# Performance work log

Measured on AMD Instinct MI355X. Metric: run time of the kernel, lower is better.

The kernel has to match this reference:

```python
import jax, jax.numpy as jnp
import numpy as np

EPS = 1e-8  # torch F.cosine_similarity default eps
NEG_INF = jnp.float32(-1e30)


def setup_inputs() -> dict:
    key = jax.random.key(0)
    k1, k2 = jax.random.split(key)
    N, M, D = 65536, 1024, 256
    embeddings = jax.random.normal(k1, (N, D), dtype=jnp.float32)
    prototypes = jax.random.normal(k2, (M, D), dtype=jnp.float32)
    counts = jnp.ones((M,), dtype=jnp.int64)  # all categories active
    return {"embeddings": embeddings, "prototypes": prototypes, "counts": counts}


def reference(embeddings, prototypes, counts):
    # Cosine similarity without materializing [N, M, D]:
    # sim[n, m] = <e_n, p_m> / max(||e_n|| * ||p_m||, eps)
    e_norm = jnp.linalg.norm(embeddings, axis=-1)            # [N]
    p_norm = jnp.linalg.norm(prototypes, axis=-1)            # [M]
    dots = jnp.einsum("nd,md->nm", embeddings, prototypes)   # [N, M]
    sim = dots / jnp.maximum(e_norm[:, None] * p_norm[None, :], EPS)
    # Mask inactive prototypes (counts == 0), matching `prototypes[active]`.
    active = counts > 0                                       # [M]
    sim = jnp.where(active[None, :], sim, NEG_INF)
    return jnp.argmax(sim, axis=-1)                           # [N] int
```

## Files before the change

### kernel.cpp

```cpp
#include <hip/hip_runtime.h>
#include <hip/hip_bf16.h>

typedef _Float16 f16x8 __attribute__((ext_vector_type(8)));
typedef float f32x4 __attribute__((ext_vector_type(4)));

#define TAU_Q 164
#define MASK_Q 2098790u

typedef const __attribute__((address_space(1))) void gas_void;
typedef __attribute__((address_space(3))) void las_void;

__device__ __forceinline__ void gload_lds16(const void* g, void* l) {
  __builtin_amdgcn_global_load_lds((gas_void*)g, (las_void*)l, 16, 0, 0);
}

__global__ __launch_bounds__(64) void prep_kernel(
    const float* __restrict__ P, const int* __restrict__ counts,
    float* __restrict__ q, int* __restrict__ wcount, f16x8* __restrict__ bhi) {
  const int m = blockIdx.x, lane = threadIdx.x;
  if (m == 0 && lane == 0) *wcount = 0;
  float4 v = *reinterpret_cast<const float4*>(P + (size_t)m * 256 + lane * 4);
  float s = v.x * v.x + v.y * v.y + v.z * v.z + v.w * v.w;
  for (int off = 32; off > 0; off >>= 1) s += __shfl_xor(s, off, 64);
  const float qm = (counts[m] > 0) ? (1.0f / sqrtf(s)) : 0.0f;
  if (lane == 0) q[m] = qm;
  if (lane < 32) {
    const int kg = lane;
    const float* src = P + (size_t)m * 256 + kg * 8;
    float4 v0 = *reinterpret_cast<const float4*>(src);
    float4 v1 = *reinterpret_cast<const float4*>(src + 4);
    float pe[8] = {v0.x, v0.y, v0.z, v0.w, v1.x, v1.y, v1.z, v1.w};
    f16x8 hi;
#pragma unroll
    for (int t = 0; t < 8; ++t) hi[t] = (_Float16)(pe[t] * qm);
    const int dst = ((m >> 4) * 8 + (kg >> 2)) * 64 + (kg & 3) * 16 + (m & 15);
    bhi[dst] = hi;
  }
}

__global__ __launch_bounds__(256) void screen_kernel(
    const float* __restrict__ E, const f16x8* __restrict__ bhi,
    int* __restrict__ out, int* __restrict__ wcount,
    int* __restrict__ wl, int wlcap) {
  __shared__ __align__(16) unsigned char ldsB[32768];

  const int tid = threadIdx.x;
  const int wave = tid >> 6, lane = tid & 63;
  const int g = lane >> 4, c = lane & 15;
  const int blockRow = blockIdx.x * 128;
  const char* bhiB = (const char*)bhi;

  auto stageB = [&](int b, int ch) {
#pragma unroll
    for (int i = 0; i < 4; ++i) {
      const int j = wave * 4 + i;
      gload_lds16(bhiB + ((size_t)ch << 14) + ((size_t)j << 10) + (size_t)lane * 16,
                  (char*)ldsB + (b << 14) + (j << 10));
    }
  };

  stageB(0, 0);

  f16x8 a[2][8];
#pragma unroll
  for (int fr = 0; fr < 2; ++fr) {
    const float* rowp = E + (size_t)(blockRow + wave * 32 + fr * 16 + c) * 256 + g * 8;
#pragma unroll
    for (int kc = 0; kc < 8; ++kc) {
      const float* p = rowp + kc * 32;
      float4 v0 = *reinterpret_cast<const float4*>(p);
      float4 v1 = *reinterpret_cast<const float4*>(p + 4);
      f16x8 h;
      h[0] = (_Float16)v0.x; h[1] = (_Float16)v0.y;
      h[2] = (_Float16)v0.z; h[3] = (_Float16)v0.w;
      h[4] = (_Float16)v1.x; h[5] = (_Float16)v1.y;
      h[6] = (_Float16)v1.z; h[7] = (_Float16)v1.w;
      a[fr][kc] = h;
    }
  }
  __syncthreads();

  unsigned t1[8], t2[8];
#pragma unroll
  for (int s = 0; s < 8; ++s) { t1[s] = 0u; t2[s] = 0u; }

#pragma unroll 1
  for (int ch = 0; ch < 32; ++ch) {
    const int buf = ch & 1;
    if (ch < 31) stageB(buf ^ 1, ch + 1);

    f32x4 acc[2][2];
#pragma unroll
    for (int fr = 0; fr < 2; ++fr)
#pragma unroll
      for (int fc = 0; fc < 2; ++fc) acc[fr][fc] = (f32x4){0.f, 0.f, 0.f, 0.f};

#pragma unroll
    for (int kc = 0; kc < 8; ++kc) {
      f16x8 bf[2];
#pragma unroll
      for (int fc = 0; fc < 2; ++fc) {
        const int j = fc * 8 + kc;
        bf[fc] = *reinterpret_cast<const f16x8*>(
            (const char*)ldsB + (buf << 14) + (j << 10) + (size_t)lane * 16);
      }
#pragma unroll
      for (int fr = 0; fr < 2; ++fr)
#pragma unroll
        for (int fc = 0; fc < 2; ++fc)
          acc[fr][fc] = __builtin_amdgcn_mfma_f32_16x16x32_f16(a[fr][kc], bf[fc], acc[fr][fc], 0, 0, 0);
    }

#pragma unroll
    for (int fc = 0; fc < 2; ++fc) {
      const unsigned mp = (unsigned)(1023 - (ch * 32 + fc * 16 + c));
#pragma unroll
      for (int fr = 0; fr < 2; ++fr)
#pragma unroll
        for (int reg = 0; reg < 4; ++reg) {
          const int s = fr * 4 + reg;
          const float v = acc[fr][fc][reg];
          const unsigned k = ((unsigned)fmaf(v, 32768.0f, 2097152.0f) << 10) | mp;
          const unsigned lo = (k < t1[s]) ? k : t1[s];
          t1[s] = (k > t1[s]) ? k : t1[s];
          t2[s] = (lo > t2[s]) ? lo : t2[s];
        }
    }

    __syncthreads();
  }

#pragma unroll
  for (int s = 0; s < 8; ++s) {
#pragma unroll
    for (int off = 1; off <= 8; off <<= 1) {
      const unsigned o1 = (unsigned)__shfl_xor((int)t1[s], off);
      const unsigned o2 = (unsigned)__shfl_xor((int)t2[s], off);
      const unsigned lo = (o1 < t1[s]) ? o1 : t1[s];
      t1[s] = (o1 > t1[s]) ? o1 : t1[s];
      const unsigned hi2 = (o2 > t2[s]) ? o2 : t2[s];
      t2[s] = (lo > hi2) ? lo : hi2;
    }
  }

  if (c == 0) {
#pragma unroll
    for (int s = 0; s < 8; ++s) {
      const int grow = blockRow + wave * 32 + (s >> 2) * 16 + g * 4 + (s & 3);
      const unsigned T1 = t1[s], T2 = t2[s];
      out[grow] = 1023 - (int)(T1 & 1023u);
      const unsigned iq1 = T1 >> 10, iq2 = T2 >> 10;
      if ((int)(iq1 - iq2) < TAU_Q || iq1 < MASK_Q) {
        const int p = atomicAdd(wcount, 1);
        if (p < wlcap) wl[p] = grow;
      }
    }
  }
}

__global__ __launch_bounds__(256) void rescue_kernel(
    const float* __restrict__ E, const float* __restrict__ P,
    const float* __restrict__ q, int* __restrict__ out,
    const int* __restrict__ wcount, const int* __restrict__ wl, int wlcap) {
  __shared__ float Elds[4][260];
  __shared__ int rowsS[4];
  __shared__ float wv[4][4];
  __shared__ int wm[4][4];

  const int tid = threadIdx.x;
  const int wave = tid >> 6, lane = tid & 63;
  int total = *wcount;
  if (total > wlcap) total = wlcap;

  for (int b0 = blockIdx.x * 4; b0 < total; b0 += gridDim.x * 4) {
    const int nb = min(4, total - b0);
    __syncthreads();
    if (tid < 4) rowsS[tid] = wl[b0 + (tid < nb ? tid : 0)];
    __syncthreads();
    {
      const int r = tid >> 6, k4 = tid & 63;
      *reinterpret_cast<float4*>(&Elds[r][k4 * 4]) =
          *reinterpret_cast<const float4*>(E + (size_t)rowsS[r] * 256 + k4 * 4);
    }
    __syncthreads();

    float acc[4][4];
#pragma unroll
    for (int r = 0; r < 4; ++r)
#pragma unroll
      for (int j = 0; j < 4; ++j) acc[r][j] = 0.f;

#pragma unroll 4
    for (int k4 = 0; k4 < 64; ++k4) {
      float4 pv[4];
#pragma unroll
      for (int j = 0; j < 4; ++j)
        pv[j] = *reinterpret_cast<const float4*>(P + (size_t)(tid + 256 * j) * 256 + k4 * 4);
      float4 ev[4];
#pragma unroll
      for (int r = 0; r < 4; ++r) ev[r] = *reinterpret_cast<const float4*>(&Elds[r][k4 * 4]);
#pragma unroll
      for (int r = 0; r < 4; ++r)
#pragma unroll
        for (int j = 0; j < 4; ++j) {
          float a = acc[r][j];
          a = fmaf(pv[j].x, ev[r].x, a);
          a = fmaf(pv[j].y, ev[r].y, a);
          a = fmaf(pv[j].z, ev[r].z, a);
          a = fmaf(pv[j].w, ev[r].w, a);
          acc[r][j] = a;
        }
    }

    float qv[4];
#pragma unroll
    for (int j = 0; j < 4; ++j) qv[j] = q[tid + 256 * j];

#pragma unroll
    for (int r = 0; r < 4; ++r) {
      float bv = -3.0e38f;
      int bm = 0;
#pragma unroll
      for (int j = 0; j < 4; ++j) {
        const float v = (qv[j] > 0.f) ? acc[r][j] * qv[j] : -1.0e30f;
        if (v > bv) { bv = v; bm = tid + 256 * j; }
      }
#pragma unroll
      for (int off = 1; off <= 32; off <<= 1) {
        const float ov = __shfl_xor(bv, off);
        const int om = __shfl_xor(bm, off);
        if (ov > bv || (ov == bv && om < bm)) { bv = ov; bm = om; }
      }
      if (lane == 0) { wv[r][wave] = bv; wm[r][wave] = bm; }
    }
    __syncthreads();
    if (tid < 4) {
      float bv = wv[tid][0];
      int bm = wm[tid][0];
#pragma unroll
      for (int w = 1; w < 4; ++w) {
        const float ov = wv[tid][w];
        const int om = wm[tid][w];
        if (ov > bv || (ov == bv && om < bm)) { bv = ov; bm = om; }
      }
      if (tid < nb) out[rowsS[tid]] = bm;
    }
    __syncthreads();
  }
}

extern "C" void kernel_launch(void* const* d_in, const int* in_sizes, int n_in,
                              void* d_out, int out_size, void* d_ws, size_t ws_size,
                              hipStream_t stream) {
  const float* E = (const float*)d_in[0];
  const float* P = (const float*)d_in[1];
  const int* counts = (const int*)d_in[2];
  const int M = in_sizes[2];
  const int Dd = in_sizes[1] / M;
  const int N = in_sizes[0] / Dd;
  int* out = (int*)d_out;

  float* qv = (float*)d_ws;
  int* wcount = (int*)((char*)d_ws + 4096);
  f16x8* bhi = (f16x8*)((char*)d_ws + 8192);
  int* wl = (int*)((char*)d_ws + 8192 + 524288);
  long long cap = ((long long)ws_size - (8192 + 524288)) / 4;
  if (cap < 0) cap = 0;
  if (cap > N) cap = N;
  int wlcap = (int)cap;

  prep_kernel<<<M, 64, 0, stream>>>(P, counts, qv, wcount, bhi);
  screen_kernel<<<N / 128, 256, 0, stream>>>(E, bhi, out, wcount, wl, wlcap);
  rescue_kernel<<<512, 256, 0, stream>>>(E, P, qv, out, wcount, wl, wlcap);
}
```

Measured before the change: 104.7 us.

## Split screen block into 2x2 wave grid over rows and prototype columns

The screen kernel now handles 64 rows per block instead of 128. The four waves form a 2x2 grid: two row groups, each split across two prototype column halves. The block count doubles to raise occupancy and parallelism across CUs. Each wave issues half as many MFMAs per chunk. The per-column top-2 partial results are then merged through LDS before the output and worklist write. The cost is staging the B matrix from global into LDS twice as often per row, plus an extra barrier and merge step.

```diff
diff --git a/kernel.cpp b/kernel.cpp
--- a/kernel.cpp
+++ b/kernel.cpp
@@ -46,8 +46,9 @@
 
   const int tid = threadIdx.x;
   const int wave = tid >> 6, lane = tid & 63;
+  const int rg = wave >> 1, cg = wave & 1;
   const int g = lane >> 4, c = lane & 15;
-  const int blockRow = blockIdx.x * 128;
+  const int blockRow = blockIdx.x * 64;
   const char* bhiB = (const char*)bhi;
 
   auto stageB = [&](int b, int ch) {
@@ -64,7 +65,7 @@
   f16x8 a[2][8];
 #pragma unroll
   for (int fr = 0; fr < 2; ++fr) {
-    const float* rowp = E + (size_t)(blockRow + wave * 32 + fr * 16 + c) * 256 + g * 8;
+    const float* rowp = E + (size_t)(blockRow + rg * 32 + fr * 16 + c) * 256 + g * 8;
 #pragma unroll
     for (int kc = 0; kc < 8; ++kc) {
       const float* p = rowp + kc * 32;
@@ -89,37 +90,28 @@
     const int buf = ch & 1;
     if (ch < 31) stageB(buf ^ 1, ch + 1);
 
-    f32x4 acc[2][2];
-#pragma unroll
-    for (int fr = 0; fr < 2; ++fr)
-#pragma unroll
-      for (int fc = 0; fc < 2; ++fc) acc[fr][fc] = (f32x4){0.f, 0.f, 0.f, 0.f};
+    f32x4 acc[2];
+#pragma unroll
+    for (int fr = 0; fr < 2; ++fr) acc[fr] = (f32x4){0.f, 0.f, 0.f, 0.f};
 
 #pragma unroll
     for (int kc = 0; kc < 8; ++kc) {
-      f16x8 bf[2];
-#pragma unroll
-      for (int fc = 0; fc < 2; ++fc) {
-        const int j = fc * 8 + kc;
-        bf[fc] = *reinterpret_cast<const f16x8*>(
-            (const char*)ldsB + (buf << 14) + (j << 10) + (size_t)lane * 16);
-      }
+      const int j = cg * 8 + kc;
+      const f16x8 bf = *reinterpret_cast<const f16x8*>(
+          (const char*)ldsB + (buf << 14) + (j << 10) + (size_t)lane * 16);
 #pragma unroll
       for (int fr = 0; fr < 2; ++fr)
-#pragma unroll
-        for (int fc = 0; fc < 2; ++fc)
-          acc[fr][fc] = __builtin_amdgcn_mfma_f32_16x16x32_f16(a[fr][kc], bf[fc], acc[fr][fc], 0, 0, 0);
-    }
-
-#pragma unroll
-    for (int fc = 0; fc < 2; ++fc) {
-      const unsigned mp = (unsigned)(1023 - (ch * 32 + fc * 16 + c));
+        acc[fr] = __builtin_amdgcn_mfma_f32_16x16x32_f16(a[fr][kc], bf, acc[fr], 0, 0, 0);
+    }
+
+    {
+      const unsigned mp = (unsigned)(1023 - (ch * 32 + cg * 16 + c));
 #pragma unroll
       for (int fr = 0; fr < 2; ++fr)
 #pragma unroll
         for (int reg = 0; reg < 4; ++reg) {
           const int s = fr * 4 + reg;
-          const float v = acc[fr][fc][reg];
+          const float v = acc[fr][reg];
           const unsigned k = ((unsigned)fmaf(v, 32768.0f, 2097152.0f) << 10) | mp;
           const unsigned lo = (k < t1[s]) ? k : t1[s];
           t1[s] = (k > t1[s]) ? k : t1[s];
@@ -143,17 +135,29 @@
     }
   }
 
+  unsigned* mg = reinterpret_cast<unsigned*>(ldsB);
   if (c == 0) {
 #pragma unroll
     for (int s = 0; s < 8; ++s) {
-      const int grow = blockRow + wave * 32 + (s >> 2) * 16 + g * 4 + (s & 3);
-      const unsigned T1 = t1[s], T2 = t2[s];
-      out[grow] = 1023 - (int)(T1 & 1023u);
-      const unsigned iq1 = T1 >> 10, iq2 = T2 >> 10;
-      if ((int)(iq1 - iq2) < TAU_Q || iq1 < MASK_Q) {
-        const int p = atomicAdd(wcount, 1);
-        if (p < wlcap) wl[p] = grow;
-      }
+      const int row = rg * 32 + (s >> 2) * 16 + g * 4 + (s & 3);
+      mg[(row * 2 + cg) * 2 + 0] = t1[s];
+      mg[(row * 2 + cg) * 2 + 1] = t2[s];
+    }
+  }
+  __syncthreads();
+  if (tid < 64) {
+    const unsigned a1v = mg[(tid * 2 + 0) * 2 + 0], a2v = mg[(tid * 2 + 0) * 2 + 1];
+    const unsigned b1v = mg[(tid * 2 + 1) * 2 + 0], b2v = mg[(tid * 2 + 1) * 2 + 1];
+    const unsigned lo = (a1v < b1v) ? a1v : b1v;
+    const unsigned T1 = (a1v > b1v) ? a1v : b1v;
+    unsigned T2 = (a2v > b2v) ? a2v : b2v;
+    T2 = (lo > T2) ? lo : T2;
+    const int grow = blockRow + tid;
+    out[grow] = 1023 - (int)(T1 & 1023u);
+    const unsigned iq1 = T1 >> 10, iq2 = T2 >> 10;
+    if ((int)(iq1 - iq2) < TAU_Q || iq1 < MASK_Q) {
+      const int p = atomicAdd(wcount, 1);
+      if (p < wlcap) wl[p] = grow;
     }
   }
 }
@@ -270,6 +274,6 @@
   int wlcap = (int)cap;
 
   prep_kernel<<<M, 64, 0, stream>>>(P, counts, qv, wcount, bhi);
-  screen_kernel<<<N / 128, 256, 0, stream>>>(E, bhi, out, wcount, wl, wlcap);
+  screen_kernel<<<N / 64, 256, 0, stream>>>(E, bhi, out, wcount, wl, wlcap);
   rescue_kernel<<<512, 256, 0, stream>>>(E, P, qv, out, wcount, wl, wlcap);
 }
```

After: 107.7 us. +2.9%, slower.
